# Kernel optimization log

Hardware: AMD Instinct MI355X
Metric: run time of the kernel (lower is better)

## Reference

```python
import jax, jax.numpy as jnp
import numpy as np

B, S = 8, 2048
E1, E2, E3 = 256, 256, 512
E = E1 + E2 + E3
NEG_SLOPE = 0.2


def setup_inputs() -> dict:
    key = jax.random.key(0)
    ks = jax.random.split(key, 11)
    scale = 1.0 / np.sqrt(E)
    return {
        "embeding1": jax.random.normal(ks[0], (B, S, E1), jnp.float32),
        "embeding2": jax.random.normal(ks[1], (B, S, E2), jnp.float32),
        "embeding3": jax.random.normal(ks[2], (B, S, E3), jnp.float32),
        # nn.Linear weights are [out, in]; apply as x @ W.T + b
        "Wq": jax.random.uniform(ks[3], (E, E), jnp.float32, -scale, scale),
        "bq": jax.random.uniform(ks[4], (E,), jnp.float32, -scale, scale),
        "Wk": jax.random.uniform(ks[5], (E, E), jnp.float32, -scale, scale),
        "bk": jax.random.uniform(ks[6], (E,), jnp.float32, -scale, scale),
        "Wv": jax.random.uniform(ks[7], (E, E), jnp.float32, -scale, scale),
        "bv": jax.random.uniform(ks[8], (E,), jnp.float32, -scale, scale),
        "Wf": jax.random.uniform(ks[9], (E, E), jnp.float32, -scale, scale),
        "bf": jax.random.uniform(ks[10], (E,), jnp.float32, -scale, scale),
    }


def reference(embeding1, embeding2, embeding3, Wq, bq, Wk, bk, Wv, bv, Wf, bf):
    x = jnp.concatenate([embeding1, embeding2, embeding3], axis=-1)  # [B,S,E]
    q = jnp.einsum("bse,oe->bso", x, Wq) + bq
    k = jnp.einsum("bse,oe->bso", x, Wk) + bk
    v = jnp.einsum("bse,oe->bso", x, Wv) + bv
    # NOTE: no 1/sqrt(d) scaling, faithful to the original module
    scores = jnp.einsum("bqe,bke->bqk", q, k)  # [B,S,S]
    probs = jax.nn.softmax(scores, axis=-1)
    weighted = jnp.einsum("bqk,bke->bqe", probs, v)  # [B,S,E]
    out = jnp.einsum("bse,oe->bso", weighted, Wf) + bf
    return jnp.where(out >= 0, out, NEG_SLOPE * out)
```

## Files before the change

kernel.cpp:

```cpp
#include <hip/hip_runtime.h>
#include <hip/hip_fp16.h>

typedef _Float16 half8 __attribute__((ext_vector_type(8)));
typedef _Float16 half4v __attribute__((ext_vector_type(4)));
typedef float floatx4 __attribute__((ext_vector_type(4)));

__device__ __forceinline__ void load_lds16(const void* g, void* l) {
    __builtin_amdgcn_global_load_lds(
        (const __attribute__((address_space(1))) void*)g,
        (__attribute__((address_space(3))) void*)l,
        16, 0, 0);
}

__device__ __forceinline__ void stage_half(const _Float16* g, long ld, _Float16* dst) {
    const int t = threadIdx.x;
#pragma unroll
    for (int j = 0; j < 2; ++j) {
        const int c = j * 512 + t;
        const int row = c >> 3;
        const int slot = (c & 7) ^ (row & 7);
        load_lds16(g + (long)row * ld + slot * 8, dst + c * 8);
    }
}

#define GEMM_PRELUDE                                                               \
    const int lane = threadIdx.x & 63;                                             \
    const int w    = threadIdx.x >> 6;                                             \
    const int wr   = w >> 2;                                                       \
    const int wc   = w & 3;                                                        \
    const int rsel = lane & 15, gsel = lane >> 4;                                  \
    const int NT = K >> 6;                                                         \
    (void)lane;
#define STAGE(BUF, KT)                                                             \
    stage_half(A + (KT) * 64, lda, lds + (BUF) * 32768);                           \
    stage_half(A + (long)128 * lda + (KT) * 64, lda, lds + (BUF) * 32768 + 8192);  \
    stage_half(B + (KT) * 64, ldb, lds + (BUF) * 32768 + 16384);                   \
    stage_half(B + (long)128 * ldb + (KT) * 64, ldb, lds + (BUF) * 32768 + 24576);
#define READ_A(dst, AH, MH)                                                        \
    _Pragma("unroll") for (int mi = 0; mi < 4; ++mi) {                             \
        const int r = ((MH) * 4 + mi) * 16 + rsel;                                 \
        dst[mi][0] = *(const half8*)&(AH)[r * 64 + ((gsel ^ (r & 7)) << 3)];       \
        dst[mi][1] = *(const half8*)&(AH)[r * 64 + (((4 + gsel) ^ (r & 7)) << 3)]; \
    }
#define READ_B(dst, BH, NH)                                                        \
    _Pragma("unroll") for (int ni = 0; ni < 2; ++ni) {                             \
        const int rn = (wc & 1) * 64 + ((NH) * 2 + ni) * 16 + rsel;                \
        dst[ni][0] = *(const half8*)&(BH)[rn * 64 + ((gsel ^ (rn & 7)) << 3)];     \
        dst[ni][1] = *(const half8*)&(BH)[rn * 64 + (((4 + gsel) ^ (rn & 7)) << 3)]; \
    }
#define MFMA_Q(MH, NH, A_, B_)                                                     \
    _Pragma("unroll") for (int mi = 0; mi < 4; ++mi)                               \
    _Pragma("unroll") for (int ni = 0; ni < 2; ++ni) {                             \
        acc[(MH) * 4 + mi][(NH) * 2 + ni] = __builtin_amdgcn_mfma_f32_16x16x32_f16( \
            A_[mi][0], B_[ni][0], acc[(MH) * 4 + mi][(NH) * 2 + ni], 0, 0, 0);     \
        acc[(MH) * 4 + mi][(NH) * 2 + ni] = __builtin_amdgcn_mfma_f32_16x16x32_f16( \
            A_[mi][1], B_[ni][1], acc[(MH) * 4 + mi][(NH) * 2 + ni], 0, 0, 0);     \
    }
#define SB0 __builtin_amdgcn_sched_barrier(0)

__device__ __forceinline__ void gemm256_core(const _Float16* A, long lda,
                                             const _Float16* B, long ldb,
                                             int K, floatx4 acc[8][4],
                                             _Float16* lds) {
    GEMM_PRELUDE
    half8 a_lo[4][2], a_hi[4][2], b_lo[2][2], b_hi[2][2];
    STAGE(0, 0);
    asm volatile("s_waitcnt vmcnt(0)" ::: "memory");
    __builtin_amdgcn_s_barrier();
    SB0;
#pragma unroll 1
    for (int t = 0; t < NT; ++t) {
        const int buf = t & 1;
        if (t + 1 < NT) { STAGE(buf ^ 1, t + 1); }
        const _Float16* Ah = lds + buf * 32768 + wr * 8192;
        const _Float16* Bh = lds + buf * 32768 + 16384 + (wc >> 1) * 8192;
        READ_A(a_lo, Ah, 0);
        READ_B(b_lo, Bh, 0);
        SB0;
        READ_A(a_hi, Ah, 1);
        SB0;
        READ_B(b_hi, Bh, 1);
        asm volatile("s_waitcnt lgkmcnt(12)" ::: "memory");
        SB0;
        MFMA_Q(0, 0, a_lo, b_lo);
        asm volatile("s_waitcnt lgkmcnt(4)" ::: "memory");
        SB0;
        MFMA_Q(1, 0, a_hi, b_lo);
        asm volatile("s_waitcnt lgkmcnt(0)" ::: "memory");
        SB0;
        MFMA_Q(0, 1, a_lo, b_hi);
        MFMA_Q(1, 1, a_hi, b_hi);
        asm volatile("s_waitcnt vmcnt(0)" ::: "memory");
        __builtin_amdgcn_s_barrier();
        SB0;
    }
}

__device__ __forceinline__ void gemm256_core_pv(const _Float16* A, long lda,
                                                const _Float16* B, long ldb,
                                                int K, floatx4 acc[8][4],
                                                _Float16* lds, const float* scl) {
    GEMM_PRELUDE
    half8 a_lo[4][2], a_hi[4][2], b_lo[2][2], b_hi[2][2];
    STAGE(0, 0);
    asm volatile("s_waitcnt vmcnt(0)" ::: "memory");
    __builtin_amdgcn_s_barrier();
    SB0;
#pragma unroll 1
    for (int t = 0; t < NT; ++t) {
        const int buf = t & 1;
        if (t + 1 < NT) { STAGE(buf ^ 1, t + 1); }
        const _Float16* Ah = lds + buf * 32768 + wr * 8192;
        const _Float16* Bh = lds + buf * 32768 + 16384 + (wc >> 1) * 8192;
        const float* srow = scl + (t >> 2) * 256 + wr * 128 + rsel;
        float s_lo[4], s_hi[4];
#pragma unroll
        for (int mi = 0; mi < 4; ++mi) s_lo[mi] = srow[mi * 16];
#pragma unroll
        for (int mi = 0; mi < 4; ++mi) s_hi[mi] = srow[64 + mi * 16];
        SB0;
        READ_A(a_lo, Ah, 0);
        READ_B(b_lo, Bh, 0);
        SB0;
        READ_A(a_hi, Ah, 1);
        SB0;
        READ_B(b_hi, Bh, 1);
        asm volatile("s_waitcnt lgkmcnt(12)" ::: "memory");
        SB0;
#pragma unroll
        for (int mi = 0; mi < 4; ++mi) {
            const _Float16 h = (_Float16)s_lo[mi];
            a_lo[mi][0] = a_lo[mi][0] * h;
            a_lo[mi][1] = a_lo[mi][1] * h;
        }
        MFMA_Q(0, 0, a_lo, b_lo);
        asm volatile("s_waitcnt lgkmcnt(4)" ::: "memory");
        SB0;
#pragma unroll
        for (int mi = 0; mi < 4; ++mi) {
            const _Float16 h = (_Float16)s_hi[mi];
            a_hi[mi][0] = a_hi[mi][0] * h;
            a_hi[mi][1] = a_hi[mi][1] * h;
        }
        MFMA_Q(1, 0, a_hi, b_lo);
        asm volatile("s_waitcnt lgkmcnt(0)" ::: "memory");
        SB0;
        MFMA_Q(0, 1, a_lo, b_hi);
        MFMA_Q(1, 1, a_hi, b_hi);
        asm volatile("s_waitcnt vmcnt(0)" ::: "memory");
        __builtin_amdgcn_s_barrier();
        SB0;
    }
}

__device__ __forceinline__ void zero_acc8(floatx4 acc[8][4]) {
    const floatx4 z = {0.f, 0.f, 0.f, 0.f};
#pragma unroll
    for (int m = 0; m < 8; ++m)
#pragma unroll
        for (int n = 0; n < 4; ++n) acc[m][n] = z;
}


__global__ __launch_bounds__(256) void prep_kernel(const float* e1, const float* e2,
                                                   const float* e3, const float* Wq,
                                                   const float* Wk, const float* Wv,
                                                   const float* Wf, _Float16* X,
                                                   _Float16* Wdst) {
    const int bid = blockIdx.x;
    if (bid < 16384) {
        long i = ((long)bid * 256 + threadIdx.x) * 4;
        int m = (int)(i >> 10);
        int c = (int)(i & 1023);
        const float* src;
        if (c < 256)      src = e1 + (long)m * 256 + c;
        else if (c < 512) src = e2 + (long)m * 256 + (c - 256);
        else              src = e3 + (long)m * 512 + (c - 512);
        float4 f = *(const float4*)src;
        half4v h;
        h[0] = (_Float16)f.x; h[1] = (_Float16)f.y;
        h[2] = (_Float16)f.z; h[3] = (_Float16)f.w;
        *(half4v*)&X[i] = h;
    } else {
        long i = ((long)(bid - 16384) * 256 + threadIdx.x) * 4;
        int which = (int)(i >> 20);
        long off = i & 1048575;
        const float* w = which == 0 ? Wq : which == 1 ? Wk : which == 2 ? Wv : Wf;
        float4 f = *(const float4*)(w + off);
        half4v h;
        h[0] = (_Float16)f.x; h[1] = (_Float16)f.y;
        h[2] = (_Float16)f.z; h[3] = (_Float16)f.w;
        *(half4v*)&Wdst[i] = h;
    }
}

__global__ __launch_bounds__(512, 2) void qkv_kernel(const _Float16* X, const _Float16* W,
                                                     const float* bq, const float* bk,
                                                     const float* bv, _Float16* q,
                                                     _Float16* k, _Float16* vT) {
    extern __shared__ _Float16 lds[];
    const int m0 = blockIdx.x * 256;
    const int n0 = blockIdx.y * 256;
    const int z  = blockIdx.z;
    floatx4 acc[8][4];
    zero_acc8(acc);
    gemm256_core(X + (long)m0 * 1024, 1024,
                 W + (long)z * 1048576 + (long)n0 * 1024, 1024, 1024, acc, lds);

    const float* bias = (z == 0) ? bq : (z == 1) ? bk : bv;
    const int lane = threadIdx.x & 63;
    const int w = threadIdx.x >> 6;
    const int wr = w >> 2, wc = w & 3;
    const int rsel = lane & 15, gsel = lane >> 4;

    if (z == 2) {
        const int rb = wr * 128 + gsel * 4;
        const int cb = wc * 64 + rsel;
#pragma unroll
        for (int mI = 0; mI < 8; ++mI) {
#pragma unroll
            for (int nI = 0; nI < 4; ++nI) {
                const int c = cb + nI * 16;
                const int r = rb + mI * 16;
                const float bb = bias[n0 + c];
                half4v vv;
#pragma unroll
                for (int j = 0; j < 4; ++j) vv[j] = (_Float16)(acc[mI][nI][j] + bb);
                *(half4v*)&lds[c * 256 + (r ^ ((c & 7) << 3))] = vv;
            }
        }
        __syncthreads();
#pragma unroll
        for (int it = 0; it < 16; ++it) {
            const int idx = it * 512 + threadIdx.x;
            const int c = idx >> 5;
            const int mc = idx & 31;
            half8 v = *(const half8*)&lds[c * 256 + ((mc * 8) ^ ((c & 7) << 3))];
            *(half8*)&vT[(long)(n0 + c) * 16384 + m0 + mc * 8] = v;
        }
    } else {
        _Float16* dst = (z == 0) ? q : k;
        const int r0 = m0 + wr * 128 + gsel * 4;
        const int c0 = n0 + wc * 64 + rsel;
#pragma unroll
        for (int mI = 0; mI < 8; ++mI) {
#pragma unroll
            for (int nI = 0; nI < 4; ++nI) {
                const int r = r0 + mI * 16;
                const int c = c0 + nI * 16;
                const float bb = bias[c];
#pragma unroll
                for (int j = 0; j < 4; ++j)
                    dst[(long)(r + j) * 1024 + c] = (_Float16)(acc[mI][nI][j] + bb);
            }
        }
    }
}

__global__ __launch_bounds__(512, 2) void scores_kernel(const _Float16* qh,
                                                        const _Float16* kh,
                                                        _Float16* es, float* tmax,
                                                        float* tsum) {
    extern __shared__ _Float16 lds[];
    const int b = blockIdx.x;
    const int m0 = (blockIdx.y >> 3) * 256;
    const int tile = blockIdx.y & 7;
    const int n0 = tile * 256;
    floatx4 acc[8][4];
    zero_acc8(acc);
    gemm256_core(qh + ((long)b * 2048 + m0) * 1024, 1024,
                 kh + ((long)b * 2048 + n0) * 1024, 1024, 1024, acc, lds);

    const int lane = threadIdx.x & 63;
    const int w = threadIdx.x >> 6;
    const int wr = w >> 2, wc = w & 3;
    const int rsel = lane & 15, gsel = lane >> 4;
    const int tid = threadIdx.x;
    float* redp   = (float*)(lds + 32768);
    float* rowmax = (float*)(lds + 67584);
    const int slot = wc * 16 + rsel;

#pragma unroll
    for (int m = 0; m < 8; ++m) {
#pragma unroll
        for (int j = 0; j < 4; ++j) {
            const int row = wr * 128 + m * 16 + gsel * 4 + j;
            float v = acc[m][0][j];
#pragma unroll
            for (int n = 1; n < 4; ++n) v = fmaxf(v, acc[m][n][j]);
            redp[row * 68 + slot] = v;
        }
    }
    __syncthreads();

    if (tid < 256) {
        const float* rr = redp + tid * 68;
        float mv = -1e30f;
#pragma unroll
        for (int q4 = 0; q4 < 16; ++q4) {
            float4 f = ((const float4*)rr)[q4];
            mv = fmaxf(mv, fmaxf(fmaxf(f.x, f.y), fmaxf(f.z, f.w)));
        }
        rowmax[tid] = mv;
    }
    __syncthreads();

#pragma unroll
    for (int m = 0; m < 8; ++m) {
#pragma unroll
        for (int j = 0; j < 4; ++j) {
            const int row = wr * 128 + m * 16 + gsel * 4 + j;
            const float mxv = rowmax[row];
            float s = 0.f;
#pragma unroll
            for (int n = 0; n < 4; ++n) {
                float e = __expf(acc[m][n][j] - mxv);
                acc[m][n][j] = e;
                s += e;
            }
            redp[row * 68 + slot] = s;
        }
    }
#pragma unroll
    for (int m = 0; m < 4; ++m) {
#pragma unroll
        for (int j = 0; j < 4; ++j) {
            const int lr = wr * 64 + m * 16 + gsel * 4 + j;
            const int g = lr & 7;
#pragma unroll
            for (int n = 0; n < 4; ++n) {
                const int c = wc * 64 + n * 16 + rsel;
                lds[lr * 256 + (c ^ (g << 3))] = (_Float16)acc[m][n][j];
            }
        }
    }
    __syncthreads();

    if (tid < 256) {
        const float* rr = redp + tid * 68;
        float sv = 0.f;
#pragma unroll
        for (int q4 = 0; q4 < 16; ++q4) {
            float4 f = ((const float4*)rr)[q4];
            sv += f.x + f.y + f.z + f.w;
        }
        const long base = ((long)b * 8 + tile) * 2048 + m0;
        tmax[base + tid] = rowmax[tid];
        tsum[base + tid] = sv;
    }
    const long rbase = (long)b * 2048 * 2048;
#pragma unroll
    for (int it = 0; it < 8; ++it) {
        const int idx = it * 512 + tid;
        const int lr = idx >> 5;
        const int chunk = idx & 31;
        half8 v = *(const half8*)&lds[lr * 256 + ((chunk ^ (lr & 7)) * 8)];
        const int rg = (lr & 63) + ((lr >> 6) << 7);
        *(half8*)&es[rbase + (long)(m0 + rg) * 2048 + n0 + chunk * 8] = v;
    }
    __syncthreads();

#pragma unroll
    for (int m = 4; m < 8; ++m) {
#pragma unroll
        for (int j = 0; j < 4; ++j) {
            const int lr = wr * 64 + (m - 4) * 16 + gsel * 4 + j;
            const int g = lr & 7;
#pragma unroll
            for (int n = 0; n < 4; ++n) {
                const int c = wc * 64 + n * 16 + rsel;
                lds[lr * 256 + (c ^ (g << 3))] = (_Float16)acc[m][n][j];
            }
        }
    }
    __syncthreads();
#pragma unroll
    for (int it = 0; it < 8; ++it) {
        const int idx = it * 512 + tid;
        const int lr = idx >> 5;
        const int chunk = idx & 31;
        half8 v = *(const half8*)&lds[lr * 256 + ((chunk ^ (lr & 7)) * 8)];
        const int rg = 64 + (lr & 63) + ((lr >> 6) << 7);
        *(half8*)&es[rbase + (long)(m0 + rg) * 2048 + n0 + chunk * 8] = v;
    }
}

__global__ __launch_bounds__(512, 2) void pv_kernel(const _Float16* es,
                                                    const _Float16* vT,
                                                    const float* tmax,
                                                    const float* tsum,
                                                    _Float16* wt) {
    extern __shared__ _Float16 lds[];
    const int batch = blockIdx.x;
    const int m0 = (blockIdx.y >> 2) * 256;
    const int n0 = (blockIdx.y & 3) * 256;
    float* scl = (float*)(lds + 65536);
    if (threadIdx.x < 256) {
        const int row = m0 + threadIdx.x;
        float m[8];
        float mg = -1e30f;
#pragma unroll
        for (int t = 0; t < 8; ++t) {
            m[t] = tmax[((long)batch * 8 + t) * 2048 + row];
            mg = fmaxf(mg, m[t]);
        }
        float Z = 0.f;
#pragma unroll
        for (int t = 0; t < 8; ++t)
            Z += tsum[((long)batch * 8 + t) * 2048 + row] * __expf(m[t] - mg);
        const float inv = 1.0f / Z;
#pragma unroll
        for (int t = 0; t < 8; ++t)
            scl[t * 256 + threadIdx.x] = __expf(m[t] - mg) * inv;
    }
    __syncthreads();
    floatx4 acc[8][4];
    zero_acc8(acc);
    gemm256_core_pv(es + ((long)batch * 2048 + m0) * 2048, 2048,
                    vT + (long)n0 * 16384 + (long)batch * 2048, 16384, 2048, acc,
                    lds, scl);

    const int lane = threadIdx.x & 63;
    const int w = threadIdx.x >> 6;
    const int wr = w >> 2, wc = w & 3;
    const int r0 = wr * 128 + (lane >> 4) * 4;
    const int c0 = n0 + wc * 64 + (lane & 15);
#pragma unroll
    for (int m = 0; m < 8; ++m) {
#pragma unroll
        for (int n = 0; n < 4; ++n) {
            const int r = r0 + m * 16;
            const int c = c0 + n * 16;
#pragma unroll
            for (int j = 0; j < 4; ++j)
                wt[((long)batch * 2048 + m0 + r + j) * 1024 + c] =
                    (_Float16)acc[m][n][j];
        }
    }
}

__global__ __launch_bounds__(512, 2) void out_kernel(const _Float16* wt, const _Float16* Wf,
                                                     const float* bf_, float* out) {
    extern __shared__ _Float16 lds[];
    const int m0 = blockIdx.x * 256;
    const int n0 = blockIdx.y * 256;
    floatx4 acc[8][4];
    zero_acc8(acc);
    gemm256_core(wt + (long)m0 * 1024, 1024, Wf + (long)n0 * 1024, 1024, 1024, acc, lds);

    const int lane = threadIdx.x & 63;
    const int w = threadIdx.x >> 6;
    const int wr = w >> 2, wc = w & 3;
    const int r0 = m0 + wr * 128 + (lane >> 4) * 4;
    const int c0 = n0 + wc * 64 + (lane & 15);
#pragma unroll
    for (int m = 0; m < 8; ++m) {
#pragma unroll
        for (int n = 0; n < 4; ++n) {
            const int r = r0 + m * 16;
            const int c = c0 + n * 16;
            const float bb = bf_[c];
#pragma unroll
            for (int j = 0; j < 4; ++j) {
                float y = acc[m][n][j] + bb;
                y = (y >= 0.f) ? y : 0.2f * y;
                out[(long)(r + j) * 1024 + c] = y;
            }
        }
    }
}

extern "C" void kernel_launch(void* const* d_in, const int* in_sizes, int n_in,
                              void* d_out, int out_size, void* d_ws, size_t ws_size,
                              hipStream_t stream) {
    const float* e1 = (const float*)d_in[0];
    const float* e2 = (const float*)d_in[1];
    const float* e3 = (const float*)d_in[2];
    const float* Wq = (const float*)d_in[3];
    const float* bq = (const float*)d_in[4];
    const float* Wk = (const float*)d_in[5];
    const float* bk = (const float*)d_in[6];
    const float* Wv = (const float*)d_in[7];
    const float* bv = (const float*)d_in[8];
    const float* Wf = (const float*)d_in[9];
    const float* bf_ = (const float*)d_in[10];
    float* out = (float*)d_out;

    const int LDS_BYTES = 131072;
    const int LDS_SC = 136192;
    const int LDS_PV = 131072 + 8192;
    (void)hipFuncSetAttribute((const void*)qkv_kernel,
                              hipFuncAttributeMaxDynamicSharedMemorySize, LDS_BYTES);
    (void)hipFuncSetAttribute((const void*)scores_kernel,
                              hipFuncAttributeMaxDynamicSharedMemorySize, LDS_SC);
    (void)hipFuncSetAttribute((const void*)pv_kernel,
                              hipFuncAttributeMaxDynamicSharedMemorySize, LDS_PV);
    (void)hipFuncSetAttribute((const void*)out_kernel,
                              hipFuncAttributeMaxDynamicSharedMemorySize, LDS_BYTES);

    char* ws = (char*)d_ws;
    const size_t MB = 1024 * 1024;
    _Float16* Xh    = (_Float16*)(ws + 0);
    _Float16* Wh    = (_Float16*)(ws + 32 * MB);
    _Float16* qh    = (_Float16*)(ws + 40 * MB);
    _Float16* kh    = (_Float16*)(ws + 72 * MB);
    _Float16* vT    = (_Float16*)(ws + 104 * MB);
    _Float16* wt    = (_Float16*)(ws + 136 * MB);
    _Float16* es    = (_Float16*)(ws + 168 * MB);
    float* tmax     = (float*)(ws + 232 * MB);
    float* tsum     = (float*)(ws + 232 * MB + 524288);

    prep_kernel<<<20480, 256, 0, stream>>>(e1, e2, e3, Wq, Wk, Wv, Wf, Xh, Wh);
    qkv_kernel<<<dim3(64, 4, 3), 512, LDS_BYTES, stream>>>(Xh, Wh, bq, bk, bv, qh, kh, vT);
    scores_kernel<<<dim3(8, 64), 512, LDS_SC, stream>>>(qh, kh, es, tmax, tsum);
    pv_kernel<<<dim3(8, 32), 512, LDS_PV, stream>>>(es, vT, tmax, tsum, wt);
    out_kernel<<<dim3(64, 4), 512, LDS_BYTES, stream>>>(wt, Wh + 3 * 1048576, bf_, out);
}
```

Baseline: 296.1 us.

## Use 8-phase ping-pong pipelined GEMM core for QKV projection

Adds a new GEMM mainloop that splits each K-tile into four MFMA phases separated by barriers, staging half-tiles of A and B into the alternate LDS buffer between phases, with setprio raised around MFMA bursts. The QKV kernel switches to this core. The aim is finer interleaving of global-to-LDS loads with matrix math so load latency hides behind compute. In exchange it adds many more barriers per tile, and it relies on hand-tuned waitcnt values that could stall or race if they are wrong.

```diff
diff --git a/kernel.cpp b/kernel.cpp
--- a/kernel.cpp
+++ b/kernel.cpp
@@ -94,6 +94,76 @@
         __builtin_amdgcn_s_barrier();
         SB0;
     }
+}
+
+__device__ __forceinline__ void gemm256_core8(const _Float16* A, long lda,
+                                              const _Float16* B, long ldb,
+                                              int K, floatx4 acc[8][4],
+                                              _Float16* lds) {
+    const int lane = threadIdx.x & 63;
+    const int w = threadIdx.x >> 6;
+    const int wr = w >> 2, wc = w & 3;
+    const int rsel = lane & 15, gsel = lane >> 4;
+    const int NT = K >> 6, NI = NT >> 1;
+    (void)lane;
+
+#define ASL(BUF, H) (lds + (BUF) * 32768 + (H) * 8192)
+#define BSL(BUF, H) (lds + (BUF) * 32768 + 16384 + (H) * 8192)
+#define STG_A(BUF, H, KT) stage_half(A + (long)(H) * 128 * lda + (KT) * 64, lda, ASL(BUF, H))
+#define STG_B(BUF, H, KT) stage_half(B + (long)(H) * 128 * ldb + (KT) * 64, ldb, BSL(BUF, H))
+#define PH(MH, NH, A_, B_)                                         \
+    __builtin_amdgcn_s_barrier();                                  \
+    asm volatile("s_waitcnt lgkmcnt(0)" ::: "memory");             \
+    __builtin_amdgcn_sched_barrier(0);                             \
+    __builtin_amdgcn_s_setprio(1);                                 \
+    MFMA_Q(MH, NH, A_, B_);                                        \
+    __builtin_amdgcn_s_setprio(0);                                 \
+    __builtin_amdgcn_s_barrier();
+
+    half8 a_lo[4][2], a_hi[4][2], b_lo[2][2], b_hi[2][2];
+
+    STG_A(0, 0, 0); STG_A(0, 1, 0); STG_B(0, 0, 0); STG_B(0, 1, 0);
+    STG_A(1, 0, 1); STG_A(1, 1, 1);
+    asm volatile("s_waitcnt vmcnt(4)" ::: "memory");
+    __builtin_amdgcn_s_barrier();
+
+#pragma unroll 1
+    for (int i = 0; i < NI; ++i) {
+        const int t1 = 2 * i + 1;
+        const int s2 = (2 * i + 2 < NT) ? 2 * i + 2 : NT - 1;
+        const int s3 = (2 * i + 3 < NT) ? 2 * i + 3 : NT - 1;
+        const _Float16* Ah0 = ASL(0, wr);
+        const _Float16* Bh0 = BSL(0, wc >> 1);
+        const _Float16* Ah1 = ASL(1, wr);
+        const _Float16* Bh1 = BSL(1, wc >> 1);
+        READ_A(a_lo, Ah0, 0); READ_B(b_lo, Bh0, 0); STG_B(1, 0, t1);
+        asm volatile("s_waitcnt lgkmcnt(8)" ::: "memory");
+        PH(0, 0, a_lo, b_lo);
+        READ_A(a_hi, Ah0, 1); STG_B(1, 1, t1);
+        PH(1, 0, a_hi, b_lo);
+        READ_B(b_hi, Bh0, 1); STG_A(0, 0, s2);
+        PH(0, 1, a_lo, b_hi);
+        STG_A(0, 1, s2);
+        asm volatile("s_waitcnt vmcnt(4)" ::: "memory");
+        PH(1, 1, a_hi, b_hi);
+        READ_A(a_lo, Ah1, 0); READ_B(b_lo, Bh1, 0); STG_B(0, 0, s2);
+        asm volatile("s_waitcnt lgkmcnt(8)" ::: "memory");
+        PH(0, 0, a_lo, b_lo);
+        READ_A(a_hi, Ah1, 1); STG_B(0, 1, s2);
+        PH(1, 0, a_hi, b_lo);
+        READ_B(b_hi, Bh1, 1); STG_A(1, 0, s3);
+        PH(0, 1, a_lo, b_hi);
+        STG_A(1, 1, s3);
+        asm volatile("s_waitcnt vmcnt(4)" ::: "memory");
+        PH(1, 1, a_hi, b_hi);
+    }
+    asm volatile("s_waitcnt vmcnt(0)" ::: "memory");
+    __builtin_amdgcn_s_barrier();
+#undef ASL
+#undef BSL
+#undef STG_A
+#undef STG_B
+#undef PH
 }
 
 __device__ __forceinline__ void gemm256_core_pv(const _Float16* A, long lda,
@@ -204,8 +274,8 @@
     const int z  = blockIdx.z;
     floatx4 acc[8][4];
     zero_acc8(acc);
-    gemm256_core(X + (long)m0 * 1024, 1024,
-                 W + (long)z * 1048576 + (long)n0 * 1024, 1024, 1024, acc, lds);
+    gemm256_core8(X + (long)m0 * 1024, 1024,
+                  W + (long)z * 1048576 + (long)n0 * 1024, 1024, 1024, acc, lds);
 
     const float* bias = (z == 0) ? bq : (z == 1) ? bk : bv;
     const int lane = threadIdx.x & 63;
```

New measurement: 307.5 us. 1.04x slower.
